# Kernel optimization log

Measured on AMD Instinct MI355X. Metric: run time of the kernel, lower is better.

## Reference

```python
import jax, jax.numpy as jnp
import numpy as np

B, CIN, COUT, K, L = 16, 512, 512, 3, 8192
STRIDE, PAD, DIL = 1, 1, 1  # 'same' conv: Lout == L


def setup_inputs() -> dict:
    key = jax.random.key(0)
    k1, k2, k3 = jax.random.split(key, 3)
    x = jax.random.normal(k1, (B, CIN, L), dtype=jnp.float32)
    # int8 quantized weight stored as int32 for portability; values in [-128, 127]
    qweight = jax.random.randint(k2, (COUT, CIN, K), -128, 128, dtype=jnp.int32)
    scale = jnp.float32(0.01)  # per-tensor dequant scale (w_max / 127)
    bias = jax.random.normal(k3, (COUT,), dtype=jnp.float32)
    return {"x": x, "qweight": qweight, "scale": scale, "bias": bias}


def reference(x, qweight, scale, bias):
    # Dequantize: fp32 weight = int8 * scale (materialized every call, as in torch module)
    w = (qweight.astype(jnp.float32) * scale).astype(x.dtype)
    out = jax.lax.conv_general_dilated(
        x, w,
        window_strides=(STRIDE,),
        padding=[(PAD, PAD)],
        rhs_dilation=(DIL,),
        dimension_numbers=("NCH", "OIH", "NCH"),
        feature_group_count=1,
    )
    return out + bias.astype(x.dtype)[None, :, None]
```

## Files before the change

kernel.cpp:

```cpp
#include <hip/hip_runtime.h>
#include <hip/hip_bf16.h>

#define CIN   512
#define COUT  512
#define LEN   8192
#define NB    16
#define KW    3
#define PROWS 8200

#define WB_ELEMS (COUT * CIN * KW)
#define WB_BYTES ((size_t)WB_ELEMS * 2)
#define PLANEB   ((size_t)PROWS * 16)
#define XS_BYTES ((size_t)NB * 8 * 8 * PLANEB)

#define XPREP_BLOCKS (NB * 8 * (LEN / 64))
#define WCONV_BLOCKS ((WB_ELEMS + 255) / 256)

#define BM2 256
#define BN2 256
#define BK3 64
#define NT  24

typedef __attribute__((ext_vector_type(4)))  float f32x4;
typedef __attribute__((ext_vector_type(16))) float f32x16;
typedef __attribute__((ext_vector_type(8)))  short bf16x8;

static __device__ __forceinline__ unsigned short f2bf(float f) {
    union { float f; unsigned u; } cv; cv.f = f;
    return (unsigned short)((cv.u + 0x7fffu + ((cv.u >> 16) & 1u)) >> 16);
}

__global__ __launch_bounds__(256) void prep_kernel(const float* __restrict__ x,
                                                   const int* __restrict__ q,
                                                   char* __restrict__ xs2,
                                                   char* __restrict__ wb2) {
    __shared__ char T[64 * 132];
    int blk = blockIdx.x;
    int tid = threadIdx.x;

    if (blk >= XPREP_BLOCKS) {
        int idx = (blk - XPREP_BLOCKS) * 256 + tid;
        if (idx < WB_ELEMS) {
            int co  = idx / (CIN * KW);
            int rem = idx - co * (CIN * KW);
            int ci  = rem / KW;
            int t   = rem - ci * KW;
            unsigned short v = f2bf((float)q[idx]);
            int cc = (ci >> 6) * KW + t;
            size_t byte = ((size_t)(co >> 8) * NT + cc) * 32768
                        + (size_t)((ci >> 3) & 7) * 4096
                        + (size_t)(co & 255) * 16 + (ci & 7) * 2;
            *(unsigned short*)(wb2 + byte) = v;
        }
        return;
    }

    int b   = blk >> 10;
    int q8  = (blk >> 7) & 7;
    int l0  = (blk & 127) * 64;
    char* xp = xs2 + ((size_t)(b * 8 + q8) * 8) * PLANEB;

    if (l0 == 0 && tid < 8) {
        f32x4 z = {};
        *(f32x4*)(xp + (size_t)tid * PLANEB) = z;
    }
    if (l0 == (LEN - 64) && tid < 8) {
        f32x4 z = {};
        *(f32x4*)(xp + (size_t)tid * PLANEB + (size_t)(LEN + 1) * 16) = z;
    }

    const float* src = x + ((size_t)b * CIN + q8 * 64) * LEN + l0;
    for (int i = tid; i < 64 * 16; i += 256) {
        int r = i >> 4, c4 = i & 15;
        f32x4 v = *(const f32x4*)(src + (size_t)r * LEN + c4 * 4);
        unsigned lo = (unsigned)f2bf(v[0]) | ((unsigned)f2bf(v[1]) << 16);
        unsigned hi = (unsigned)f2bf(v[2]) | ((unsigned)f2bf(v[3]) << 16);
        char* p = T + r * 132 + c4 * 8;
        *(unsigned*)p       = lo;
        *(unsigned*)(p + 4) = hi;
    }
    __syncthreads();
    for (int i = tid; i < 64 * 8; i += 256) {
        int l = i >> 3, c8 = i & 7;
        union { bf16x8 v; unsigned short s[8]; } pk;
        #pragma unroll
        for (int j = 0; j < 8; ++j)
            pk.s[j] = *(const unsigned short*)(T + (c8 * 8 + j) * 132 + l * 2);
        *(bf16x8*)(xp + (size_t)c8 * PLANEB + (size_t)(1 + l0 + l) * 16) = pk.v;
    }
}

__global__ __launch_bounds__(512, 2) void conv_kernel(
    const char* __restrict__ xs2,
    const char* __restrict__ wb2,
    const float* __restrict__ scale_p,
    const float* __restrict__ bias,
    float* __restrict__ out)
{
    __shared__ char sA[2][32768];
    __shared__ char sB[2][32768];

    const int bid = blockIdx.x;
    const int logical = (bid & 7) * 128 + (bid >> 3);
    const int co_tile = logical & 1;
    const int l_tile  = logical >> 1;
    const int b   = l_tile >> 5;
    const int l0  = (l_tile & 31) * BN2;
    const int co0 = co_tile * BM2;

    const int tid  = threadIdx.x;
    const int lane = tid & 63;
    const int wid  = tid >> 6;
    const int wr   = wid >> 2;
    const int wc   = wid & 3;
    const int la   = lane & 31;
    const int lh   = lane >> 5;

    f32x16 acc[4][2] = {};

    const char* wbA  = wb2 + (size_t)co_tile * NT * 32768;
    const char* xs2b = xs2 + (size_t)b * 8 * 8 * PLANEB + (size_t)l0 * 16;

    const int ldsW = wid * 4096 + lane * 16;
    const size_t bS0 = (size_t)wid * PLANEB + lane * 16;

    const char* pAr = &sA[0][0] + lh * 4096 + wr * 512 + la * 16;
    const char* pBr = &sB[0][0] + lh * 4096 + wc * 1024 + la * 16;

#define BAR()    __builtin_amdgcn_s_barrier()
#define SCHED0() __builtin_amdgcn_sched_barrier(0)
#define LGKM0()  asm volatile("s_waitcnt lgkmcnt(0)" ::: "memory")

#define GL(src_, dst_) __builtin_amdgcn_global_load_lds(                                     \
    (const __attribute__((address_space(1))) unsigned int*)(src_),                           \
    (__attribute__((address_space(3))) unsigned int*)(dst_), 16, 0, 0)

#define STAGEU(buf_, c_, u_) do {                                                            \
    int tap_ = (c_) % KW;  int q_ = (c_) / KW;                                               \
    if ((u_) < 2) {                                                                          \
        const char* s_ = xs2b + (size_t)q_ * (8 * PLANEB) + bS0                              \
                         + (size_t)(tap_ + (u_) * 128) * 16;                                 \
        char* d_ = &sB[buf_][0] + ldsW + (u_) * 2048;                                        \
        GL(s_, d_);  GL(s_ + 1024, d_ + 1024);                                               \
    } else {                                                                                 \
        const char* s_ = wbA + (size_t)(c_) * 32768 + ldsW + ((u_) & 1) * 2048;              \
        char* d_ = &sA[buf_][0] + ldsW + ((u_) & 1) * 2048;                                  \
        GL(s_, d_);  GL(s_ + 1024, d_ + 1024);                                               \
    } } while (0)

#define LDA(d_, buf_, mb_, s_) d_ = *(const bf16x8*)(pAr + (buf_) * 32768 + (s_) * 8192 + (mb_) * 1024)
#define LDB(d_, buf_, nb_, s_) d_ = *(const bf16x8*)(pBr + (buf_) * 32768 + (s_) * 8192 + (nb_) * 512)

#define MFMA8(MB_, B00_, B01_, B10_, B11_) do {                                              \
    __builtin_amdgcn_s_setprio(1);                                                           \
    acc[(MB_)  ][0] = __builtin_amdgcn_mfma_f32_32x32x16_bf16(a0_, B00_, acc[(MB_)  ][0],0,0,0); \
    acc[(MB_)  ][1] = __builtin_amdgcn_mfma_f32_32x32x16_bf16(a0_, B01_, acc[(MB_)  ][1],0,0,0); \
    acc[(MB_)+1][0] = __builtin_amdgcn_mfma_f32_32x32x16_bf16(a2_, B00_, acc[(MB_)+1][0],0,0,0); \
    acc[(MB_)+1][1] = __builtin_amdgcn_mfma_f32_32x32x16_bf16(a2_, B01_, acc[(MB_)+1][1],0,0,0); \
    acc[(MB_)  ][0] = __builtin_amdgcn_mfma_f32_32x32x16_bf16(a1_, B10_, acc[(MB_)  ][0],0,0,0); \
    acc[(MB_)  ][1] = __builtin_amdgcn_mfma_f32_32x32x16_bf16(a1_, B11_, acc[(MB_)  ][1],0,0,0); \
    acc[(MB_)+1][0] = __builtin_amdgcn_mfma_f32_32x32x16_bf16(a3_, B10_, acc[(MB_)+1][0],0,0,0); \
    acc[(MB_)+1][1] = __builtin_amdgcn_mfma_f32_32x32x16_bf16(a3_, B11_, acc[(MB_)+1][1],0,0,0); \
    __builtin_amdgcn_s_setprio(0);                                                           \
    } while (0)

    STAGEU(0, 0, 0); STAGEU(0, 0, 1); STAGEU(0, 0, 2); STAGEU(0, 0, 3);
    asm volatile("s_waitcnt vmcnt(2)" ::: "memory");
    BAR();

    bf16x8 b00, b01, b10, b11, b20, b21, b30, b31;
    bf16x8 a0_, a1_, a2_, a3_;

    #pragma unroll 1
    for (int c = 0; c < NT - 1; ++c) {
        const int buf = c & 1, nb = buf ^ 1;
        SCHED0();
        LDB(b00, buf, 0, 0); LDB(b01, buf, 1, 0);
        LDB(b10, buf, 0, 1); LDB(b11, buf, 1, 1);
        LDB(b20, buf, 0, 2); LDB(b21, buf, 1, 2);
        LDB(b30, buf, 0, 3); LDB(b31, buf, 1, 3);
        LDA(a0_, buf, 0, 0); LDA(a1_, buf, 0, 1); LDA(a2_, buf, 1, 0); LDA(a3_, buf, 1, 1);
        STAGEU(nb, c + 1, 0);
        BAR(); LGKM0(); SCHED0();
        MFMA8(0, b00, b01, b10, b11);
        SCHED0();
        LDA(a0_, buf, 0, 2); LDA(a1_, buf, 0, 3); LDA(a2_, buf, 1, 2); LDA(a3_, buf, 1, 3);
        STAGEU(nb, c + 1, 1);
        asm volatile("s_waitcnt vmcnt(4)" ::: "memory");
        BAR(); LGKM0(); SCHED0();
        MFMA8(0, b20, b21, b30, b31);
        SCHED0();
        LDA(a0_, buf, 2, 0); LDA(a1_, buf, 2, 1); LDA(a2_, buf, 3, 0); LDA(a3_, buf, 3, 1);
        STAGEU(nb, c + 1, 2);
        BAR(); LGKM0(); SCHED0();
        MFMA8(2, b00, b01, b10, b11);
        SCHED0();
        LDA(a0_, buf, 2, 2); LDA(a1_, buf, 2, 3); LDA(a2_, buf, 3, 2); LDA(a3_, buf, 3, 3);
        STAGEU(nb, c + 1, 3);
        asm volatile("s_waitcnt vmcnt(2)" ::: "memory");
        BAR(); LGKM0(); SCHED0();
        MFMA8(2, b20, b21, b30, b31);
    }
    {
        const int buf = (NT - 1) & 1;
        SCHED0();
        LDB(b00, buf, 0, 0); LDB(b01, buf, 1, 0);
        LDB(b10, buf, 0, 1); LDB(b11, buf, 1, 1);
        LDB(b20, buf, 0, 2); LDB(b21, buf, 1, 2);
        LDB(b30, buf, 0, 3); LDB(b31, buf, 1, 3);
        LDA(a0_, buf, 0, 0); LDA(a1_, buf, 0, 1); LDA(a2_, buf, 1, 0); LDA(a3_, buf, 1, 1);
        BAR(); LGKM0(); SCHED0();
        MFMA8(0, b00, b01, b10, b11);
        SCHED0();
        LDA(a0_, buf, 0, 2); LDA(a1_, buf, 0, 3); LDA(a2_, buf, 1, 2); LDA(a3_, buf, 1, 3);
        asm volatile("s_waitcnt vmcnt(0)" ::: "memory");
        BAR(); LGKM0(); SCHED0();
        MFMA8(0, b20, b21, b30, b31);
        SCHED0();
        LDA(a0_, buf, 2, 0); LDA(a1_, buf, 2, 1); LDA(a2_, buf, 3, 0); LDA(a3_, buf, 3, 1);
        BAR(); LGKM0(); SCHED0();
        MFMA8(2, b00, b01, b10, b11);
        SCHED0();
        LDA(a0_, buf, 2, 2); LDA(a1_, buf, 2, 3); LDA(a2_, buf, 3, 2); LDA(a3_, buf, 3, 3);
        LGKM0(); SCHED0();
        MFMA8(2, b20, b21, b30, b31);
    }
#undef STAGEU
#undef LDA
#undef LDB
#undef MFMA8
#undef GL

    const float sc = scale_p[0];
    #pragma unroll
    for (int mb = 0; mb < 4; ++mb) {
        const int coB = co0 + mb * 64 + wr * 32 + 4 * lh;
        #pragma unroll
        for (int rg = 0; rg < 16; ++rg) {
            int co = coB + (rg & 3) + 8 * (rg >> 2);
            float bv = bias[co];
            size_t orow = ((size_t)b * COUT + co) * LEN + l0 + wc * 64 + la;
            out[orow]      = sc * acc[mb][0][rg] + bv;
            out[orow + 32] = sc * acc[mb][1][rg] + bv;
        }
    }
}

__global__ __launch_bounds__(256) void wconv_kernel(const int* __restrict__ q,
                                                    unsigned short* __restrict__ wb) {
    int idx = blockIdx.x * 256 + threadIdx.x;
    if (idx >= WB_ELEMS) return;
    int co = idx / (KW * CIN);
    int r  = idx - co * (KW * CIN);
    int t  = r >> 9;
    int ci = r & 511;
    wb[idx] = f2bf((float)q[(co * CIN + ci) * KW + t]);
}

__global__ __launch_bounds__(256, 2) void conv_fb_kernel(
    const float* __restrict__ x,
    const unsigned short* __restrict__ wb,
    const float* __restrict__ scale_p,
    const float* __restrict__ bias,
    float* __restrict__ out)
{
    __shared__ char xT[132 * 128];
    const int bid = blockIdx.x;
    const int logical = (bid & 7) * 512 + (bid >> 3);
    const int co_tile = logical & 3;
    const int n_tile  = logical >> 2;
    const int b   = n_tile >> 6;
    const int l0  = (n_tile & 63) * 128;
    const int co0 = co_tile * 128;
    const int tid  = threadIdx.x;
    const int lane = tid & 63;
    const int wid  = tid >> 6;
    const int wr = wid >> 1, wc = wid & 1;
    const int lhi = lane >> 4;
    const int llo = lane & 15;
    f32x4 acc[4][4] = {};
    const float* xb = x + (size_t)b * CIN * LEN;

    for (int ci0 = 0; ci0 < CIN; ci0 += 64) {
        __syncthreads();
        for (int it = tid; it < 132 * 8; it += 256) {
            int c = it % 132;
            int o = it / 132;
            int l = l0 - 1 + c;
            float v[8];
            if (l >= 0 && l < LEN) {
                const float* src = xb + (size_t)(ci0 + o * 8) * LEN + l;
                #pragma unroll
                for (int j = 0; j < 8; ++j) v[j] = src[(size_t)j * LEN];
            } else {
                #pragma unroll
                for (int j = 0; j < 8; ++j) v[j] = 0.f;
            }
            union { bf16x8 v8; unsigned short s[8]; } pk;
            #pragma unroll
            for (int j = 0; j < 8; ++j) pk.s[j] = f2bf(v[j]);
            int byte = c * 128 + ((o * 16) ^ ((c & 7) << 4));
            *reinterpret_cast<bf16x8*>(xT + byte) = pk.v8;
        }
        __syncthreads();
        #pragma unroll
        for (int t = 0; t < KW; ++t) {
            #pragma unroll
            for (int s = 0; s < 2; ++s) {
                bf16x8 af[4];
                #pragma unroll
                for (int m = 0; m < 4; ++m)
                    af[m] = *reinterpret_cast<const bf16x8*>(
                        wb + (size_t)(co0 + wr * 64 + m * 16 + llo) * (KW * CIN)
                           + t * CIN + ci0 + s * 32 + 8 * lhi);
                bf16x8 bfr[4];
                #pragma unroll
                for (int n = 0; n < 4; ++n) {
                    int col = wc * 64 + n * 16 + llo + t;
                    int byte = col * 128 + (((s * 32 + 8 * lhi) * 2) ^ ((col & 7) << 4));
                    bfr[n] = *reinterpret_cast<const bf16x8*>(xT + byte);
                }
                #pragma unroll
                for (int m = 0; m < 4; ++m)
                    #pragma unroll
                    for (int n = 0; n < 4; ++n)
                        acc[m][n] = __builtin_amdgcn_mfma_f32_16x16x32_bf16(af[m], bfr[n], acc[m][n], 0, 0, 0);
            }
        }
    }
    const float sc = scale_p[0];
    #pragma unroll
    for (int m = 0; m < 4; ++m) {
        #pragma unroll
        for (int j = 0; j < 4; ++j) {
            int co = co0 + wr * 64 + m * 16 + lhi * 4 + j;
            float bv = bias[co];
            size_t orow = ((size_t)b * COUT + co) * LEN + l0 + wc * 64;
            #pragma unroll
            for (int n = 0; n < 4; ++n)
                out[orow + n * 16 + llo] = sc * acc[m][n][j] + bv;
        }
    }
}

extern "C" void kernel_launch(void* const* d_in, const int* in_sizes, int n_in,
                              void* d_out, int out_size, void* d_ws, size_t ws_size,
                              hipStream_t stream) {
    const float* x    = (const float*)d_in[0];
    const int*   qw   = (const int*)d_in[1];
    const float* sc   = (const float*)d_in[2];
    const float* bias = (const float*)d_in[3];
    float* out = (float*)d_out;

    if (ws_size >= WB_BYTES + XS_BYTES) {
        char* wb2 = (char*)d_ws;
        char* xs2 = (char*)d_ws + WB_BYTES;
        prep_kernel<<<XPREP_BLOCKS + WCONV_BLOCKS, 256, 0, stream>>>(x, qw, xs2, wb2);
        conv_kernel<<<(COUT / BM2) * (NB * LEN / BN2), 512, 0, stream>>>(xs2, wb2, sc, bias, out);
    } else {
        unsigned short* wb = (unsigned short*)d_ws;
        wconv_kernel<<<WCONV_BLOCKS, 256, 0, stream>>>(qw, wb);
        conv_fb_kernel<<<4096, 256, 0, stream>>>(x, wb, sc, bias, out);
    }
}
```

Before: 298.6 us.

## Fuse input bf16 conversion into conv kernel, reuse one panel across three taps

Removes the separate pass that transposed and converted the fp32 input into a padded bf16 workspace. The conv kernel now loads fp32 input straight from global memory into registers, converts it to bf16 and writes it into a 258-row LDS panel. All three kernel taps then read that panel at shifted row offsets, so each input channel group is fetched once instead of three times. In exchange, LDS use grows enough that launch bounds drop to one block per CU, and the uncoalesced strided fp32 loads plus register conversion now sit inside the MFMA pipeline.

```diff
diff --git a/kernel.cpp b/kernel.cpp
--- a/kernel.cpp
+++ b/kernel.cpp
@@ -6,22 +6,17 @@
 #define LEN   8192
 #define NB    16
 #define KW    3
-#define PROWS 8200
 
 #define WB_ELEMS (COUT * CIN * KW)
 #define WB_BYTES ((size_t)WB_ELEMS * 2)
-#define PLANEB   ((size_t)PROWS * 16)
-#define XS_BYTES ((size_t)NB * 8 * 8 * PLANEB)
-
-#define XPREP_BLOCKS (NB * 8 * (LEN / 64))
 #define WCONV_BLOCKS ((WB_ELEMS + 255) / 256)
 
-#define BM2 256
-#define BN2 256
-#define BK3 64
-#define NT  24
+#define NT   24
+#define PNLP 4128
+#define PNLB (8 * PNLP)
 
 typedef __attribute__((ext_vector_type(4)))  float f32x4;
+typedef __attribute__((ext_vector_type(8)))  float f32x8;
 typedef __attribute__((ext_vector_type(16))) float f32x16;
 typedef __attribute__((ext_vector_type(8)))  short bf16x8;
 
@@ -30,83 +25,39 @@
     return (unsigned short)((cv.u + 0x7fffu + ((cv.u >> 16) & 1u)) >> 16);
 }
 
-__global__ __launch_bounds__(256) void prep_kernel(const float* __restrict__ x,
-                                                   const int* __restrict__ q,
-                                                   char* __restrict__ xs2,
-                                                   char* __restrict__ wb2) {
-    __shared__ char T[64 * 132];
-    int blk = blockIdx.x;
-    int tid = threadIdx.x;
-
-    if (blk >= XPREP_BLOCKS) {
-        int idx = (blk - XPREP_BLOCKS) * 256 + tid;
-        if (idx < WB_ELEMS) {
-            int co  = idx / (CIN * KW);
-            int rem = idx - co * (CIN * KW);
-            int ci  = rem / KW;
-            int t   = rem - ci * KW;
-            unsigned short v = f2bf((float)q[idx]);
-            int cc = (ci >> 6) * KW + t;
-            size_t byte = ((size_t)(co >> 8) * NT + cc) * 32768
-                        + (size_t)((ci >> 3) & 7) * 4096
-                        + (size_t)(co & 255) * 16 + (ci & 7) * 2;
-            *(unsigned short*)(wb2 + byte) = v;
-        }
-        return;
-    }
-
-    int b   = blk >> 10;
-    int q8  = (blk >> 7) & 7;
-    int l0  = (blk & 127) * 64;
-    char* xp = xs2 + ((size_t)(b * 8 + q8) * 8) * PLANEB;
-
-    if (l0 == 0 && tid < 8) {
-        f32x4 z = {};
-        *(f32x4*)(xp + (size_t)tid * PLANEB) = z;
-    }
-    if (l0 == (LEN - 64) && tid < 8) {
-        f32x4 z = {};
-        *(f32x4*)(xp + (size_t)tid * PLANEB + (size_t)(LEN + 1) * 16) = z;
-    }
-
-    const float* src = x + ((size_t)b * CIN + q8 * 64) * LEN + l0;
-    for (int i = tid; i < 64 * 16; i += 256) {
-        int r = i >> 4, c4 = i & 15;
-        f32x4 v = *(const f32x4*)(src + (size_t)r * LEN + c4 * 4);
-        unsigned lo = (unsigned)f2bf(v[0]) | ((unsigned)f2bf(v[1]) << 16);
-        unsigned hi = (unsigned)f2bf(v[2]) | ((unsigned)f2bf(v[3]) << 16);
-        char* p = T + r * 132 + c4 * 8;
-        *(unsigned*)p       = lo;
-        *(unsigned*)(p + 4) = hi;
-    }
-    __syncthreads();
-    for (int i = tid; i < 64 * 8; i += 256) {
-        int l = i >> 3, c8 = i & 7;
-        union { bf16x8 v; unsigned short s[8]; } pk;
-        #pragma unroll
-        for (int j = 0; j < 8; ++j)
-            pk.s[j] = *(const unsigned short*)(T + (c8 * 8 + j) * 132 + l * 2);
-        *(bf16x8*)(xp + (size_t)c8 * PLANEB + (size_t)(1 + l0 + l) * 16) = pk.v;
-    }
-}
-
-__global__ __launch_bounds__(512, 2) void conv_kernel(
-    const char* __restrict__ xs2,
+__global__ __launch_bounds__(256) void wprep_kernel(const int* __restrict__ q,
+                                                    char* __restrict__ wb2) {
+    int idx = blockIdx.x * 256 + threadIdx.x;
+    if (idx >= WB_ELEMS) return;
+    int co  = idx / (CIN * KW);
+    int rem = idx - co * (CIN * KW);
+    int ci  = rem / KW;
+    int t   = rem - ci * KW;
+    unsigned short v = f2bf((float)q[idx]);
+    int cc = (ci >> 6) * KW + t;
+    size_t byte = ((size_t)(co >> 8) * NT + cc) * 32768
+                + (size_t)((ci >> 3) & 7) * 4096
+                + (size_t)(co & 255) * 16 + (ci & 7) * 2;
+    *(unsigned short*)(wb2 + byte) = v;
+}
+
+__global__ __launch_bounds__(512, 1) void conv_kernel(
+    const float* __restrict__ x,
     const char* __restrict__ wb2,
     const float* __restrict__ scale_p,
     const float* __restrict__ bias,
     float* __restrict__ out)
 {
     __shared__ char sA[2][32768];
-    __shared__ char sB[2][32768];
+    __shared__ char sP[2][PNLB];
 
     const int bid = blockIdx.x;
     const int logical = (bid & 7) * 128 + (bid >> 3);
     const int co_tile = logical & 1;
     const int l_tile  = logical >> 1;
     const int b   = l_tile >> 5;
-    const int l0  = (l_tile & 31) * BN2;
-    const int co0 = co_tile * BM2;
+    const int l0  = (l_tile & 31) * 256;
+    const int co0 = co_tile * 256;
 
     const int tid  = threadIdx.x;
     const int lane = tid & 63;
@@ -118,38 +69,62 @@
 
     f32x16 acc[4][2] = {};
 
-    const char* wbA  = wb2 + (size_t)co_tile * NT * 32768;
-    const char* xs2b = xs2 + (size_t)b * 8 * 8 * PLANEB + (size_t)l0 * 16;
+    const float* xb  = x + (size_t)b * CIN * LEN;
+    const char*  wbA = wb2 + (size_t)co_tile * NT * 32768;
 
     const int ldsW = wid * 4096 + lane * 16;
-    const size_t bS0 = (size_t)wid * PLANEB + lane * 16;
-
-    const char* pAr = &sA[0][0] + lh * 4096 + wr * 512 + la * 16;
-    const char* pBr = &sB[0][0] + lh * 4096 + wc * 1024 + la * 16;
+    char* const sA0 = &sA[0][0];
+    char* const sP0 = &sP[0][0];
+
+    const char* pAr = sA0 + lh * 4096 + wr * 512 + la * 16;
 
 #define BAR()    __builtin_amdgcn_s_barrier()
 #define SCHED0() __builtin_amdgcn_sched_barrier(0)
 #define LGKM0()  asm volatile("s_waitcnt lgkmcnt(0)" ::: "memory")
+#define VMC0()   asm volatile("s_waitcnt vmcnt(0)" ::: "memory")
 
 #define GL(src_, dst_) __builtin_amdgcn_global_load_lds(                                     \
     (const __attribute__((address_space(1))) unsigned int*)(src_),                           \
     (__attribute__((address_space(3))) unsigned int*)(dst_), 16, 0, 0)
 
-#define STAGEU(buf_, c_, u_) do {                                                            \
-    int tap_ = (c_) % KW;  int q_ = (c_) / KW;                                               \
-    if ((u_) < 2) {                                                                          \
-        const char* s_ = xs2b + (size_t)q_ * (8 * PLANEB) + bS0                              \
-                         + (size_t)(tap_ + (u_) * 128) * 16;                                 \
-        char* d_ = &sB[buf_][0] + ldsW + (u_) * 2048;                                        \
-        GL(s_, d_);  GL(s_ + 1024, d_ + 1024);                                               \
-    } else {                                                                                 \
-        const char* s_ = wbA + (size_t)(c_) * 32768 + ldsW + ((u_) & 1) * 2048;              \
-        char* d_ = &sA[buf_][0] + ldsW + ((u_) & 1) * 2048;                                  \
-        GL(s_, d_);  GL(s_ + 1024, d_ + 1024);                                               \
+#define AGL4(NBO_, C1_) do {                                                                 \
+    const char* s_ = wbA + (size_t)(C1_) * 32768 + ldsW;                                     \
+    char* d_ = sA0 + (NBO_) + ldsW;                                                          \
+    GL(s_, d_); GL(s_ + 1024, d_ + 1024); GL(s_ + 2048, d_ + 2048); GL(s_ + 3072, d_ + 3072);\
+    } while (0)
+
+#define BLOADU(S_, U_, XP_) do {                                                             \
+    int row_ = lane + (S_) * 64;                                                             \
+    int l_   = l0 - 1 + row_;                                                                \
+    _Pragma("unroll") for (int j_ = 0; j_ < 8; ++j_) U_[j_] = 0.f;                           \
+    if (row_ < 258 && (unsigned)l_ < (unsigned)LEN) {                                        \
+        const float* p_ = (XP_) + (size_t)(wid * 8) * LEN + l_;                              \
+        _Pragma("unroll") for (int j_ = 0; j_ < 8; ++j_) U_[j_] = p_[(size_t)j_ * LEN];      \
     } } while (0)
 
-#define LDA(d_, buf_, mb_, s_) d_ = *(const bf16x8*)(pAr + (buf_) * 32768 + (s_) * 8192 + (mb_) * 1024)
-#define LDB(d_, buf_, nb_, s_) d_ = *(const bf16x8*)(pBr + (buf_) * 32768 + (s_) * 8192 + (nb_) * 512)
+#define BPACKU(S_, U_, PW_) do {                                                             \
+    int row_ = lane + (S_) * 64;                                                             \
+    if (row_ < 258) {                                                                        \
+        union { bf16x8 v; unsigned short s[8]; } pk_;                                        \
+        _Pragma("unroll") for (int j_ = 0; j_ < 8; ++j_) pk_.s[j_] = f2bf(U_[j_]);           \
+        *(bf16x8*)((PW_) + wid * PNLP + row_ * 16) = pk_.v;                                  \
+    } } while (0)
+
+#define LDB8(PBR_, T_) do {                                                                  \
+    const char* p_ = (PBR_) + lh * PNLP + (wc * 64 + la + (T_)) * 16;                        \
+    b00 = *(const bf16x8*)(p_);               b01 = *(const bf16x8*)(p_ + 512);              \
+    b10 = *(const bf16x8*)(p_ + 8256);        b11 = *(const bf16x8*)(p_ + 8256 + 512);       \
+    b20 = *(const bf16x8*)(p_ + 16512);       b21 = *(const bf16x8*)(p_ + 16512 + 512);      \
+    b30 = *(const bf16x8*)(p_ + 24768);       b31 = *(const bf16x8*)(p_ + 24768 + 512);      \
+    } while (0)
+
+#define LDA4(BUFO_, MB_, S_) do {                                                            \
+    const char* p_ = pAr + (BUFO_);                                                          \
+    a0_ = *(const bf16x8*)(p_ + (S_) * 8192     + (MB_) * 1024);                             \
+    a1_ = *(const bf16x8*)(p_ + ((S_)+1) * 8192 + (MB_) * 1024);                             \
+    a2_ = *(const bf16x8*)(p_ + (S_) * 8192     + ((MB_)+1) * 1024);                         \
+    a3_ = *(const bf16x8*)(p_ + ((S_)+1) * 8192 + ((MB_)+1) * 1024);                         \
+    } while (0)
 
 #define MFMA8(MB_, B00_, B01_, B10_, B11_) do {                                              \
     __builtin_amdgcn_s_setprio(1);                                                           \
@@ -164,70 +139,145 @@
     __builtin_amdgcn_s_setprio(0);                                                           \
     } while (0)
 
-    STAGEU(0, 0, 0); STAGEU(0, 0, 1); STAGEU(0, 0, 2); STAGEU(0, 0, 3);
-    asm volatile("s_waitcnt vmcnt(2)" ::: "memory");
-    BAR();
-
     bf16x8 b00, b01, b10, b11, b20, b21, b30, b31;
     bf16x8 a0_, a1_, a2_, a3_;
+    f32x8 u0, u1, u2;
+
+    AGL4(0, 0);
+    BLOADU(0, u0, xb); BLOADU(1, u1, xb);
+    BPACKU(0, u0, sP0); BLOADU(2, u0, xb);
+    BPACKU(1, u1, sP0); BLOADU(3, u1, xb);
+    BPACKU(2, u0, sP0); BLOADU(4, u0, xb);
+    BPACKU(3, u1, sP0);
+    BPACKU(4, u0, sP0);
+    VMC0(); LGKM0();
+    BAR();
 
     #pragma unroll 1
-    for (int c = 0; c < NT - 1; ++c) {
-        const int buf = c & 1, nb = buf ^ 1;
-        SCHED0();
-        LDB(b00, buf, 0, 0); LDB(b01, buf, 1, 0);
-        LDB(b10, buf, 0, 1); LDB(b11, buf, 1, 1);
-        LDB(b20, buf, 0, 2); LDB(b21, buf, 1, 2);
-        LDB(b30, buf, 0, 3); LDB(b31, buf, 1, 3);
-        LDA(a0_, buf, 0, 0); LDA(a1_, buf, 0, 1); LDA(a2_, buf, 1, 0); LDA(a3_, buf, 1, 1);
-        STAGEU(nb, c + 1, 0);
-        BAR(); LGKM0(); SCHED0();
-        MFMA8(0, b00, b01, b10, b11);
-        SCHED0();
-        LDA(a0_, buf, 0, 2); LDA(a1_, buf, 0, 3); LDA(a2_, buf, 1, 2); LDA(a3_, buf, 1, 3);
-        STAGEU(nb, c + 1, 1);
-        asm volatile("s_waitcnt vmcnt(4)" ::: "memory");
-        BAR(); LGKM0(); SCHED0();
-        MFMA8(0, b20, b21, b30, b31);
-        SCHED0();
-        LDA(a0_, buf, 2, 0); LDA(a1_, buf, 2, 1); LDA(a2_, buf, 3, 0); LDA(a3_, buf, 3, 1);
-        STAGEU(nb, c + 1, 2);
-        BAR(); LGKM0(); SCHED0();
-        MFMA8(2, b00, b01, b10, b11);
-        SCHED0();
-        LDA(a0_, buf, 2, 2); LDA(a1_, buf, 2, 3); LDA(a2_, buf, 3, 2); LDA(a3_, buf, 3, 3);
-        STAGEU(nb, c + 1, 3);
-        asm volatile("s_waitcnt vmcnt(2)" ::: "memory");
-        BAR(); LGKM0(); SCHED0();
+    for (int qq = 0; qq < 7; ++qq) {
+        const int c0   = 3 * qq;
+        const int bo0  = (c0 & 1) << 15;
+        const int bo1  = bo0 ^ 32768;
+        const char* pbR = sP0 + (qq & 1) * PNLB;
+        char*       pbW = sP0 + ((qq + 1) & 1) * PNLB;
+        const float* xn = xb + (size_t)(qq + 1) * (64 * LEN);
+
+        SCHED0();
+        AGL4(bo1, c0 + 1);
+        BLOADU(0, u0, xn);
+        LDB8(pbR, 0);
+        LDA4(bo0, 0, 0);
+        BAR(); LGKM0(); SCHED0();
+        MFMA8(0, b00, b01, b10, b11);
+        SCHED0();
+        BLOADU(1, u1, xn);
+        LDA4(bo0, 0, 2);
+        BAR(); LGKM0(); SCHED0();
+        MFMA8(0, b20, b21, b30, b31);
+        SCHED0();
+        BLOADU(2, u2, xn); BPACKU(0, u0, pbW);
+        LDA4(bo0, 2, 0);
+        BAR(); LGKM0(); SCHED0();
+        MFMA8(2, b00, b01, b10, b11);
+        SCHED0();
+        BPACKU(1, u1, pbW);
+        LDA4(bo0, 2, 2);
+        BAR(); LGKM0(); SCHED0();
+        MFMA8(2, b20, b21, b30, b31);
+        SCHED0();
+        AGL4(bo0, c0 + 2);
+        BLOADU(3, u0, xn);
+        LDB8(pbR, 1);
+        LDA4(bo1, 0, 0);
+        BAR(); LGKM0(); SCHED0();
+        MFMA8(0, b00, b01, b10, b11);
+        SCHED0();
+        BLOADU(4, u1, xn); BPACKU(2, u2, pbW);
+        LDA4(bo1, 0, 2);
+        BAR(); LGKM0(); SCHED0();
+        MFMA8(0, b20, b21, b30, b31);
+        SCHED0();
+        BPACKU(3, u0, pbW);
+        LDA4(bo1, 2, 0);
+        BAR(); LGKM0(); SCHED0();
+        MFMA8(2, b00, b01, b10, b11);
+        SCHED0();
+        BPACKU(4, u1, pbW);
+        LDA4(bo1, 2, 2);
+        BAR(); LGKM0(); SCHED0();
+        MFMA8(2, b20, b21, b30, b31);
+        SCHED0();
+        AGL4(bo1, c0 + 3);
+        LDB8(pbR, 2);
+        LDA4(bo0, 0, 0);
+        BAR(); LGKM0(); SCHED0();
+        MFMA8(0, b00, b01, b10, b11);
+        SCHED0();
+        LDA4(bo0, 0, 2);
+        BAR(); LGKM0(); SCHED0();
+        MFMA8(0, b20, b21, b30, b31);
+        SCHED0();
+        LDA4(bo0, 2, 0);
+        BAR(); LGKM0(); SCHED0();
+        MFMA8(2, b00, b01, b10, b11);
+        SCHED0();
+        LDA4(bo0, 2, 2);
+        VMC0(); LGKM0();
+        BAR(); SCHED0();
         MFMA8(2, b20, b21, b30, b31);
     }
     {
-        const int buf = (NT - 1) & 1;
-        SCHED0();
-        LDB(b00, buf, 0, 0); LDB(b01, buf, 1, 0);
-        LDB(b10, buf, 0, 1); LDB(b11, buf, 1, 1);
-        LDB(b20, buf, 0, 2); LDB(b21, buf, 1, 2);
-        LDB(b30, buf, 0, 3); LDB(b31, buf, 1, 3);
-        LDA(a0_, buf, 0, 0); LDA(a1_, buf, 0, 1); LDA(a2_, buf, 1, 0); LDA(a3_, buf, 1, 1);
-        BAR(); LGKM0(); SCHED0();
-        MFMA8(0, b00, b01, b10, b11);
-        SCHED0();
-        LDA(a0_, buf, 0, 2); LDA(a1_, buf, 0, 3); LDA(a2_, buf, 1, 2); LDA(a3_, buf, 1, 3);
-        asm volatile("s_waitcnt vmcnt(0)" ::: "memory");
-        BAR(); LGKM0(); SCHED0();
-        MFMA8(0, b20, b21, b30, b31);
-        SCHED0();
-        LDA(a0_, buf, 2, 0); LDA(a1_, buf, 2, 1); LDA(a2_, buf, 3, 0); LDA(a3_, buf, 3, 1);
-        BAR(); LGKM0(); SCHED0();
-        MFMA8(2, b00, b01, b10, b11);
-        SCHED0();
-        LDA(a0_, buf, 2, 2); LDA(a1_, buf, 2, 3); LDA(a2_, buf, 3, 2); LDA(a3_, buf, 3, 3);
+        const char* pbR = sP0 + PNLB;
+        SCHED0();
+        AGL4(0, 22);
+        LDB8(pbR, 0);
+        LDA4(32768, 0, 0);
+        BAR(); LGKM0(); SCHED0();
+        MFMA8(0, b00, b01, b10, b11);
+        SCHED0(); LDA4(32768, 0, 2);
+        BAR(); LGKM0(); SCHED0();
+        MFMA8(0, b20, b21, b30, b31);
+        SCHED0(); LDA4(32768, 2, 0);
+        BAR(); LGKM0(); SCHED0();
+        MFMA8(2, b00, b01, b10, b11);
+        SCHED0(); LDA4(32768, 2, 2);
+        VMC0(); LGKM0(); BAR(); SCHED0();
+        MFMA8(2, b20, b21, b30, b31);
+        SCHED0();
+        AGL4(32768, 23);
+        LDB8(pbR, 1);
+        LDA4(0, 0, 0);
+        BAR(); LGKM0(); SCHED0();
+        MFMA8(0, b00, b01, b10, b11);
+        SCHED0(); LDA4(0, 0, 2);
+        BAR(); LGKM0(); SCHED0();
+        MFMA8(0, b20, b21, b30, b31);
+        SCHED0(); LDA4(0, 2, 0);
+        BAR(); LGKM0(); SCHED0();
+        MFMA8(2, b00, b01, b10, b11);
+        SCHED0(); LDA4(0, 2, 2);
+        VMC0(); LGKM0(); BAR(); SCHED0();
+        MFMA8(2, b20, b21, b30, b31);
+        SCHED0();
+        LDB8(pbR, 2);
+        LDA4(32768, 0, 0);
         LGKM0(); SCHED0();
-        MFMA8(2, b20, b21, b30, b31);
-    }
-#undef STAGEU
-#undef LDA
-#undef LDB
+        MFMA8(0, b00, b01, b10, b11);
+        SCHED0(); LDA4(32768, 0, 2);
+        LGKM0(); SCHED0();
+        MFMA8(0, b20, b21, b30, b31);
+        SCHED0(); LDA4(32768, 2, 0);
+        LGKM0(); SCHED0();
+        MFMA8(2, b00, b01, b10, b11);
+        SCHED0(); LDA4(32768, 2, 2);
+        LGKM0(); SCHED0();
+        MFMA8(2, b20, b21, b30, b31);
+    }
+#undef AGL4
+#undef BLOADU
+#undef BPACKU
+#undef LDB8
+#undef LDA4
 #undef MFMA8
 #undef GL
 
@@ -352,11 +402,10 @@
     const float* bias = (const float*)d_in[3];
     float* out = (float*)d_out;
 
-    if (ws_size >= WB_BYTES + XS_BYTES) {
+    if (ws_size >= WB_BYTES) {
         char* wb2 = (char*)d_ws;
-        char* xs2 = (char*)d_ws + WB_BYTES;
-        prep_kernel<<<XPREP_BLOCKS + WCONV_BLOCKS, 256, 0, stream>>>(x, qw, xs2, wb2);
-        conv_kernel<<<(COUT / BM2) * (NB * LEN / BN2), 512, 0, stream>>>(xs2, wb2, sc, bias, out);
+        wprep_kernel<<<WCONV_BLOCKS, 256, 0, stream>>>(qw, wb2);
+        conv_kernel<<<1024, 512, 0, stream>>>(x, wb2, sc, bias, out);
     } else {
         unsigned short* wb = (unsigned short*)d_ws;
         wconv_kernel<<<WCONV_BLOCKS, 256, 0, stream>>>(qw, wb);
```

Result: faster. 265.1 us (-11.2%).
